# Kernel tuning notes

Measured on AMD Instinct MI355X. Metric: run time of the kernel, lower is better.

Reference implementation:

```python
import jax, jax.numpy as jnp
import numpy as np

HID = 64
HEADS = 4
HEAD_DIM = HID // HEADS
N_MOL, N_PROT = 2048, 4096
E_MOL, E_PROT = 32768, 131072
B = 32


def _lin(key, din, dout):
    kw, kb = jax.random.split(key)
    s = 1.0 / np.sqrt(din)
    W = jax.random.uniform(kw, (din, dout), jnp.float32, -s, s)
    b = jax.random.uniform(kb, (dout,), jnp.float32, -s, s)
    return W, b


def setup_inputs() -> dict:
    key = jax.random.key(0)
    ks = jax.random.split(key, 32)
    inp = {}
    inp['mol_x'] = jax.random.normal(ks[0], (N_MOL, 11), jnp.float32)
    inp['prot_x'] = jax.random.normal(ks[1], (N_PROT, 15), jnp.float32)
    inp['mol_eattr'] = jax.random.normal(ks[2], (E_MOL, 10), jnp.float32)
    inp['prot_eattr'] = jax.random.normal(ks[3], (E_PROT, 10), jnp.float32)
    inp['mol_edge_index'] = jax.random.randint(ks[4], (2, E_MOL), 0, N_MOL, jnp.int32)
    inp['prot_edge_index'] = jax.random.randint(ks[5], (2, E_PROT), 0, N_PROT, jnp.int32)
    inp['mol_batch'] = jnp.sort(jax.random.randint(ks[6], (N_MOL,), 0, B, jnp.int32))
    inp['prot_batch'] = jnp.sort(jax.random.randint(ks[7], (N_PROT,), 0, B, jnp.int32))
    inp['node_lin_mol_W'], inp['node_lin_mol_b'] = _lin(ks[8], 11, HID)
    inp['node_lin_prot_W'], inp['node_lin_prot_b'] = _lin(ks[9], 15, HID)
    inp['edge_lin_mol_W'], inp['edge_lin_mol_b'] = _lin(ks[10], 10, HID)
    inp['edge_lin_prot_W'], inp['edge_lin_prot_b'] = _lin(ks[11], 10, HID)
    for pref, base in (('mol_conv', 12), ('prot_conv', 15)):
        W1s, b1s, W2s, b2s = [], [], [], []
        for l in range(3):
            k1, k2 = jax.random.split(ks[base + l])
            W1, b1 = _lin(k1, HID, HID)
            W2, b2 = _lin(k2, HID, HID)
            W1s.append(W1); b1s.append(b1); W2s.append(W2); b2s.append(b2)
        inp[pref + '_W1'] = jnp.stack(W1s); inp[pref + '_b1'] = jnp.stack(b1s)
        inp[pref + '_W2'] = jnp.stack(W2s); inp[pref + '_b2'] = jnp.stack(b2s)
    for pref, base in (('attn_mp', 18), ('attn_pm', 21)):
        Ws, bs = [], []
        for i in range(3):  # Q, K, V
            W, b = _lin(ks[base + i], HID, HID)
            Ws.append(W); bs.append(b)
        inp[pref + '_W'] = jnp.stack(Ws); inp[pref + '_b'] = jnp.stack(bs)
    inp['fc1_W'], inp['fc1_b'] = _lin(ks[24], 2 * HID, HID)
    inp['fc2_W'], inp['fc2_b'] = _lin(ks[25], HID, 1)
    return inp


def _gine_layer(x, src, dst, eattr, W1, b1, W2, b2):
    # message: ReLU(x_j + e_ji); GINEConv sum aggregation; eps = 0
    msg = jax.nn.relu(x[src] + eattr)                       # [E, H]
    agg = jax.ops.segment_sum(msg, dst, num_segments=x.shape[0])
    h = x + agg
    h = jax.nn.relu(h @ W1 + b1) @ W2 + b2                  # inner MLP
    return jax.nn.relu(h)                                   # post-conv ReLU


def _cross_attn(qn, kn, W, b):
    Nq, Nk = qn.shape[0], kn.shape[0]
    Q = (qn @ W[0] + b[0]).reshape(Nq, HEADS, HEAD_DIM)
    K = (kn @ W[1] + b[1]).reshape(Nk, HEADS, HEAD_DIM)
    V = (kn @ W[2] + b[2]).reshape(Nk, HEADS, HEAD_DIM)
    scores = jnp.einsum('qhd,khd->hqk', Q, K) / np.sqrt(HEAD_DIM)
    w = jax.nn.softmax(scores, axis=-1)
    out = jnp.einsum('hqk,khd->qhd', w, V)
    return out.reshape(Nq, HID)


def _pool(H, batch):
    s = jax.ops.segment_sum(H, batch, num_segments=B)
    c = jax.ops.segment_sum(jnp.ones((H.shape[0],), H.dtype), batch, num_segments=B)
    return s / jnp.maximum(c, 1.0)[:, None]


def _forward(mol_x, prot_x, mol_eattr, prot_eattr,
             node_lin_mol_W, node_lin_mol_b, node_lin_prot_W, node_lin_prot_b,
             edge_lin_mol_W, edge_lin_mol_b, edge_lin_prot_W, edge_lin_prot_b,
             mol_conv_W1, mol_conv_b1, mol_conv_W2, mol_conv_b2,
             prot_conv_W1, prot_conv_b1, prot_conv_W2, prot_conv_b2,
             attn_mp_W, attn_mp_b, attn_pm_W, attn_pm_b,
             fc1_W, fc1_b, fc2_W, fc2_b,
             mol_edge_index, prot_edge_index, mol_batch, prot_batch):
    xm = mol_x @ node_lin_mol_W + node_lin_mol_b
    xp = prot_x @ node_lin_prot_W + node_lin_prot_b
    em = mol_eattr @ edge_lin_mol_W + edge_lin_mol_b
    ep = prot_eattr @ edge_lin_prot_W + edge_lin_prot_b
    ms, md = mol_edge_index[0], mol_edge_index[1]
    ps, pd = prot_edge_index[0], prot_edge_index[1]
    for l in range(3):
        xm = _gine_layer(xm, ms, md, em, mol_conv_W1[l], mol_conv_b1[l], mol_conv_W2[l], mol_conv_b2[l])
    for l in range(3):
        xp = _gine_layer(xp, ps, pd, ep, prot_conv_W1[l], prot_conv_b1[l], prot_conv_W2[l], prot_conv_b2[l])
    H_mol = xm + _cross_attn(xm, xp, attn_mp_W, attn_mp_b)
    H_prot = xp + _cross_attn(xp, xm, attn_pm_W, attn_pm_b)
    z = jnp.concatenate([_pool(H_mol, mol_batch), _pool(H_prot, prot_batch)], axis=1)
    h = jax.nn.relu(z @ fc1_W + fc1_b)
    return jax.nn.sigmoid(h @ fc2_W + fc2_b).squeeze(-1)


def reference(mol_x, prot_x, mol_eattr, prot_eattr,
              node_lin_mol_W, node_lin_mol_b, node_lin_prot_W, node_lin_prot_b,
              edge_lin_mol_W, edge_lin_mol_b, edge_lin_prot_W, edge_lin_prot_b,
              mol_conv_W1, mol_conv_b1, mol_conv_W2, mol_conv_b2,
              prot_conv_W1, prot_conv_b1, prot_conv_W2, prot_conv_b2,
              attn_mp_W, attn_mp_b, attn_pm_W, attn_pm_b,
              fc1_W, fc1_b, fc2_W, fc2_b,
              mol_edge_index, prot_edge_index, mol_batch, prot_batch):
    return _forward(mol_x, prot_x, mol_eattr, prot_eattr,
                    node_lin_mol_W, node_lin_mol_b, node_lin_prot_W, node_lin_prot_b,
                    edge_lin_mol_W, edge_lin_mol_b, edge_lin_prot_W, edge_lin_prot_b,
                    mol_conv_W1, mol_conv_b1, mol_conv_W2, mol_conv_b2,
                    prot_conv_W1, prot_conv_b1, prot_conv_W2, prot_conv_b2,
                    attn_mp_W, attn_mp_b, attn_pm_W, attn_pm_b,
                    fc1_W, fc1_b, fc2_W, fc2_b,
                    mol_edge_index, prot_edge_index, mol_batch, prot_batch)
```

## Files before the change

### kernel.cpp

```cpp
#include <hip/hip_runtime.h>
#include <math.h>

#define HID 64
#define HEADS 4
#define HDIM 16
#define N_MOL 2048
#define N_PROT 4096
#define E_MOL 32768
#define E_PROT 131072
#define BATCH 32
#define N_TOT (N_MOL + N_PROT)
#define E_TOT (E_MOL + E_PROT)
#define CAP 128

#define TQA 16
#define TKA 32
#define KSTA 68
#define CH_MOL 4
#define CH_PROT 2
#define KCHUNK 1024
#define NGRP_MOL (N_MOL / TQA)

#define DOT4(a, b) ((a).x*(b).x + (a).y*(b).y + (a).z*(b).z + (a).w*(b).w)
#define EXP2(x) __builtin_amdgcn_exp2f(x)

__global__ void k_nlb(const float* __restrict__ mol_x, const float* __restrict__ prot_x,
                      const float* __restrict__ Wm, const float* __restrict__ bm,
                      const float* __restrict__ Wp, const float* __restrict__ bp,
                      const int* __restrict__ mol_ei, const int* __restrict__ prot_ei,
                      float* __restrict__ xm, float* __restrict__ xp,
                      int* __restrict__ cursor, int* __restrict__ eidx) {
    if (blockIdx.x < N_TOT / 4) {
        int w = threadIdx.x >> 6, t = threadIdx.x & 63;
        int n = blockIdx.x * 4 + w;
        if (n < N_MOL) {
            const float* xr = mol_x + n * 11;
            float acc = bm[t];
#pragma unroll
            for (int i = 0; i < 11; ++i) acc += xr[i] * Wm[i * HID + t];
            xm[n * HID + t] = acc;
        } else {
            int p = n - N_MOL;
            const float* xr = prot_x + p * 15;
            float acc = bp[t];
#pragma unroll
            for (int i = 0; i < 15; ++i) acc += xr[i] * Wp[i * HID + t];
            xp[p * HID + t] = acc;
        }
    } else {
        int e = (blockIdx.x - N_TOT / 4) * 256 + threadIdx.x;
        int node, loc;
        if (e < E_MOL) { node = mol_ei[E_MOL + e]; loc = e; }
        else { int el = e - E_MOL; node = N_MOL + prot_ei[E_PROT + el]; loc = el; }
        int pos = atomicAdd(&cursor[node], 1);
        eidx[(size_t)node * CAP + pos] = loc;
    }
}

__global__ void k_gine(const float* __restrict__ xin_m, const float* __restrict__ xin_p,
                       float* __restrict__ xout_m, float* __restrict__ xout_p,
                       const float* __restrict__ mol_ea, const float* __restrict__ prot_ea,
                       const int* __restrict__ mol_ei, const int* __restrict__ prot_ei,
                       const float* __restrict__ Wem, const float* __restrict__ bem,
                       const float* __restrict__ Wep, const float* __restrict__ bep,
                       const float* __restrict__ W1m, const float* __restrict__ b1m,
                       const float* __restrict__ W2m, const float* __restrict__ b2m,
                       const float* __restrict__ W1p, const float* __restrict__ b1p,
                       const float* __restrict__ W2p, const float* __restrict__ b2p,
                       const int* __restrict__ cnt, const int* __restrict__ eidx,
                       int doProj,
                       const float* __restrict__ mpW, const float* __restrict__ mpb,
                       const float* __restrict__ pmW, const float* __restrict__ pmb,
                       float* __restrict__ Qm, float* __restrict__ Kp, float* __restrict__ Vp,
                       float* __restrict__ Qp, float* __restrict__ Km, float* __restrict__ Vm) {
    __shared__ float h0[8][HID];
    __shared__ float h1[8][HID];
    int w = threadIdx.x >> 6, t = threadIdx.x & 63;
    int nb0 = blockIdx.x * 8 + w * 2;
    bool isMol = nb0 < N_MOL;
    const float* x  = isMol ? xin_m : xin_p;
    float* xo       = isMol ? xout_m : xout_p;
    const float* We = isMol ? Wem : Wep;
    float bt        = isMol ? bem[t] : bep[t];
    const float* ea_base = isMol ? mol_ea : prot_ea;
    const int* srcarr    = isMol ? mol_ei : prot_ei;
    int nbias = isMol ? 0 : N_MOL;
    float wcol[10];
#pragma unroll
    for (int i = 0; i < 10; ++i) wcol[i] = We[i * HID + t];

#pragma unroll
    for (int u = 0; u < 2; ++u) {
        int nb = nb0 + u;
        int deg = cnt[nb];
        const int* lst = eidx + (size_t)nb * CAP;
        float agg = 0.f;
        int j = 0;
        for (; j + 1 < deg; j += 2) {
            int e0 = lst[j], e1 = lst[j + 1];
            int s0 = srcarr[e0], s1 = srcarr[e1];
            const float2* p0 = (const float2*)(ea_base + (size_t)e0 * 10);
            const float2* p1 = (const float2*)(ea_base + (size_t)e1 * 10);
            float2 a0 = p0[0], a1 = p0[1], a2 = p0[2], a3 = p0[3], a4 = p0[4];
            float2 c0 = p1[0], c1 = p1[1], c2 = p1[2], c3 = p1[3], c4 = p1[4];
            float xs0 = x[s0 * HID + t];
            float xs1 = x[s1 * HID + t];
            float m0 = bt, m1 = bt;
            m0 = fmaf(a0.x, wcol[0], m0); m0 = fmaf(a0.y, wcol[1], m0);
            m0 = fmaf(a1.x, wcol[2], m0); m0 = fmaf(a1.y, wcol[3], m0);
            m0 = fmaf(a2.x, wcol[4], m0); m0 = fmaf(a2.y, wcol[5], m0);
            m0 = fmaf(a3.x, wcol[6], m0); m0 = fmaf(a3.y, wcol[7], m0);
            m0 = fmaf(a4.x, wcol[8], m0); m0 = fmaf(a4.y, wcol[9], m0);
            m1 = fmaf(c0.x, wcol[0], m1); m1 = fmaf(c0.y, wcol[1], m1);
            m1 = fmaf(c1.x, wcol[2], m1); m1 = fmaf(c1.y, wcol[3], m1);
            m1 = fmaf(c2.x, wcol[4], m1); m1 = fmaf(c2.y, wcol[5], m1);
            m1 = fmaf(c3.x, wcol[6], m1); m1 = fmaf(c3.y, wcol[7], m1);
            m1 = fmaf(c4.x, wcol[8], m1); m1 = fmaf(c4.y, wcol[9], m1);
            agg += fmaxf(m0 + xs0, 0.f) + fmaxf(m1 + xs1, 0.f);
        }
        if (j < deg) {
            int e0 = lst[j];
            int s0 = srcarr[e0];
            const float2* p0 = (const float2*)(ea_base + (size_t)e0 * 10);
            float2 a0 = p0[0], a1 = p0[1], a2 = p0[2], a3 = p0[3], a4 = p0[4];
            float xs0 = x[s0 * HID + t];
            float m0 = bt;
            m0 = fmaf(a0.x, wcol[0], m0); m0 = fmaf(a0.y, wcol[1], m0);
            m0 = fmaf(a1.x, wcol[2], m0); m0 = fmaf(a1.y, wcol[3], m0);
            m0 = fmaf(a2.x, wcol[4], m0); m0 = fmaf(a2.y, wcol[5], m0);
            m0 = fmaf(a3.x, wcol[6], m0); m0 = fmaf(a3.y, wcol[7], m0);
            m0 = fmaf(a4.x, wcol[8], m0); m0 = fmaf(a4.y, wcol[9], m0);
            agg += fmaxf(m0 + xs0, 0.f);
        }
        h0[w * 2 + u][t] = x[(nb0 - nbias + u) * HID + t] + agg;
    }

    const float* W1 = isMol ? W1m : W1p;
    const float* W2 = isMol ? W2m : W2p;
    float b1v = isMol ? b1m[t] : b1p[t];
    float b2v = isMol ? b2m[t] : b2p[t];
    float acc0 = b1v, acc1 = b1v;
    const float4* hA = (const float4*)h0[w * 2];
    const float4* hB = (const float4*)h0[w * 2 + 1];
#pragma unroll
    for (int k = 0; k < 16; ++k) {
        float4 a = hA[k], b = hB[k];
        float w0 = W1[(4 * k + 0) * HID + t], w1 = W1[(4 * k + 1) * HID + t];
        float w2 = W1[(4 * k + 2) * HID + t], w3 = W1[(4 * k + 3) * HID + t];
        acc0 = fmaf(a.x, w0, acc0); acc1 = fmaf(b.x, w0, acc1);
        acc0 = fmaf(a.y, w1, acc0); acc1 = fmaf(b.y, w1, acc1);
        acc0 = fmaf(a.z, w2, acc0); acc1 = fmaf(b.z, w2, acc1);
        acc0 = fmaf(a.w, w3, acc0); acc1 = fmaf(b.w, w3, acc1);
    }
    h1[w * 2][t] = fmaxf(acc0, 0.f);
    h1[w * 2 + 1][t] = fmaxf(acc1, 0.f);
    float d0 = b2v, d1 = b2v;
    const float4* gA = (const float4*)h1[w * 2];
    const float4* gB = (const float4*)h1[w * 2 + 1];
#pragma unroll
    for (int k = 0; k < 16; ++k) {
        float4 a = gA[k], b = gB[k];
        float w0 = W2[(4 * k + 0) * HID + t], w1 = W2[(4 * k + 1) * HID + t];
        float w2 = W2[(4 * k + 2) * HID + t], w3 = W2[(4 * k + 3) * HID + t];
        d0 = fmaf(a.x, w0, d0); d1 = fmaf(b.x, w0, d1);
        d0 = fmaf(a.y, w1, d0); d1 = fmaf(b.y, w1, d1);
        d0 = fmaf(a.z, w2, d0); d1 = fmaf(b.z, w2, d1);
        d0 = fmaf(a.w, w3, d0); d1 = fmaf(b.w, w3, d1);
    }
    int n0 = nb0 - nbias;
    float xv0 = fmaxf(d0, 0.f), xv1 = fmaxf(d1, 0.f);
    xo[n0 * HID + t] = xv0;
    xo[(n0 + 1) * HID + t] = xv1;

    if (doProj) {
        h0[w * 2][t] = xv0;
        h0[w * 2 + 1][t] = xv1;
        const float *WQ, *bQ, *WK, *bK, *WV, *bV;
        float *dQ, *dK, *dV;
        if (isMol) { WQ = mpW;        bQ = mpb;       WK = pmW + 4096; bK = pmb + 64;
                     WV = pmW + 8192; bV = pmb + 128; dQ = Qm; dK = Km; dV = Vm; }
        else       { WQ = pmW;        bQ = pmb;       WK = mpW + 4096; bK = mpb + 64;
                     WV = mpW + 8192; bV = mpb + 128; dQ = Qp; dK = Kp; dV = Vp; }
        float aQ0 = bQ[t], aQ1 = aQ0;
        float aK0 = bK[t], aK1 = aK0;
        float aV0 = bV[t], aV1 = aV0;
        const float4* rA = (const float4*)h0[w * 2];
        const float4* rB = (const float4*)h0[w * 2 + 1];
#pragma unroll
        for (int k = 0; k < 16; ++k) {
            float4 a = rA[k], b = rB[k];
#pragma unroll
            for (int j = 0; j < 4; ++j) {
                float av = (j == 0) ? a.x : (j == 1) ? a.y : (j == 2) ? a.z : a.w;
                float bv = (j == 0) ? b.x : (j == 1) ? b.y : (j == 2) ? b.z : b.w;
                float wq = WQ[(4 * k + j) * HID + t];
                float wk = WK[(4 * k + j) * HID + t];
                float wv = WV[(4 * k + j) * HID + t];
                aQ0 = fmaf(av, wq, aQ0); aQ1 = fmaf(bv, wq, aQ1);
                aK0 = fmaf(av, wk, aK0); aK1 = fmaf(bv, wk, aK1);
                aV0 = fmaf(av, wv, aV0); aV1 = fmaf(bv, wv, aV1);
            }
        }
        dQ[n0 * HID + t] = aQ0; dQ[(n0 + 1) * HID + t] = aQ1;
        dK[n0 * HID + t] = aK0; dK[(n0 + 1) * HID + t] = aK1;
        dV[n0 * HID + t] = aV0; dV[(n0 + 1) * HID + t] = aV1;
    }
}

__device__ inline void upd4(float4& A, const float4 v0, const float4 v1,
                            float p0, float p1, float al) {
    A.x = fmaf(p1, v1.x, fmaf(p0, v0.x, A.x * al));
    A.y = fmaf(p1, v1.y, fmaf(p0, v0.y, A.y * al));
    A.z = fmaf(p1, v1.z, fmaf(p0, v0.z, A.z * al));
    A.w = fmaf(p1, v1.w, fmaf(p0, v0.w, A.w * al));
}
__device__ inline void merge4(float4& A, const float4 B, float c1, float c2) {
    A.x = A.x * c1 + B.x * c2;
    A.y = A.y * c1 + B.y * c2;
    A.z = A.z * c1 + B.z * c2;
    A.w = A.w * c1 + B.w * c2;
}
__device__ inline float4 shfl4(const float4 a, int off) {
    float4 r;
    r.x = __shfl_xor(a.x, off, 64); r.y = __shfl_xor(a.y, off, 64);
    r.z = __shfl_xor(a.z, off, 64); r.w = __shfl_xor(a.w, off, 64);
    return r;
}

__global__ __launch_bounds__(256) void k_attn(
    const float* __restrict__ Qm, const float* __restrict__ Kp, const float* __restrict__ Vp,
    const float* __restrict__ Qp, const float* __restrict__ Km, const float* __restrict__ Vm,
    float* __restrict__ part_m, float* __restrict__ part_p) {
    __shared__ float Kl[2][TKA * KSTA];
    __shared__ float Vl[2][TKA * KSTA];

    int t = threadIdx.x;
    const float *Q, *K, *V;
    float* part;
    int q0, chunk, CH;
    {
        int b = blockIdx.x;
        const int MOLB = NGRP_MOL * CH_MOL;
        if (b < MOLB) {
            chunk = b & 3; q0 = (b >> 2) * TQA; CH = CH_MOL;
            Q = Qm; K = Kp; V = Vp; part = part_m;
        } else {
            b -= MOLB;
            chunk = b & 1; q0 = (b >> 1) * TQA; CH = CH_PROT;
            Q = Qp; K = Km; V = Vm; part = part_p;
        }
    }
    int kbeg = chunk * KCHUNK;

    int sub = t & 15, h = (t >> 4) & 3, qg = t >> 6;
    int r0 = t >> 4;
    int c0 = (t & 15) << 2;

    const float sc = 0.25f * 1.44269504088896f;
    float4 q4[4][4];
#pragma unroll
    for (int qq = 0; qq < 4; ++qq) {
        const float4* Qr = (const float4*)(Q + (q0 + qg * 4 + qq) * HID + h * HDIM);
#pragma unroll
        for (int j = 0; j < 4; ++j) {
            float4 v = Qr[j];
            v.x *= sc; v.y *= sc; v.z *= sc; v.w *= sc;
            q4[qq][j] = v;
        }
    }

    float mreg[4], lreg[4];
    float4 A[4][4];
#pragma unroll
    for (int qq = 0; qq < 4; ++qq) {
        mreg[qq] = -INFINITY; lreg[qq] = 0.f;
#pragma unroll
        for (int j = 0; j < 4; ++j) A[qq][j] = (float4){0.f, 0.f, 0.f, 0.f};
    }

    {
        const float4* Kg = (const float4*)(K + kbeg * HID);
        const float4* Vg = (const float4*)(V + kbeg * HID);
        float4 ka = Kg[t], kb = Kg[t + 256];
        float4 va = Vg[t], vb = Vg[t + 256];
        *(float4*)&Kl[0][r0 * KSTA + c0] = ka;
        *(float4*)&Kl[0][(r0 + 16) * KSTA + c0] = kb;
        *(float4*)&Vl[0][r0 * KSTA + c0] = va;
        *(float4*)&Vl[0][(r0 + 16) * KSTA + c0] = vb;
    }
    __syncthreads();

    const int NT = KCHUNK / TKA;
    for (int tile = 0; tile < NT; ++tile) {
        int cur = tile & 1;
        float4 ka, kb, va, vb;
        bool more = (tile + 1) < NT;
        if (more) {
            const float4* Kg = (const float4*)(K + (kbeg + (tile + 1) * TKA) * HID);
            const float4* Vg = (const float4*)(V + (kbeg + (tile + 1) * TKA) * HID);
            ka = Kg[t]; kb = Kg[t + 256];
            va = Vg[t]; vb = Vg[t + 256];
        }

        const float4* Kr0 = (const float4*)&Kl[cur][sub * KSTA + h * HDIM];
        const float4* Kr1 = (const float4*)&Kl[cur][(sub + 16) * KSTA + h * HDIM];
        float4 x0 = Kr0[0], x1 = Kr0[1], x2 = Kr0[2], x3 = Kr0[3];
        float4 y0 = Kr1[0], y1 = Kr1[1], y2 = Kr1[2], y3 = Kr1[3];

        float s0[4], s1[4];
#pragma unroll
        for (int qq = 0; qq < 4; ++qq) {
            s0[qq] = DOT4(x0, q4[qq][0]) + DOT4(x1, q4[qq][1]) + DOT4(x2, q4[qq][2]) + DOT4(x3, q4[qq][3]);
            s1[qq] = DOT4(y0, q4[qq][0]) + DOT4(y1, q4[qq][1]) + DOT4(y2, q4[qq][2]) + DOT4(y3, q4[qq][3]);
        }

        const float4* Vr0 = (const float4*)&Vl[cur][sub * KSTA + h * HDIM];
        const float4* Vr1 = (const float4*)&Vl[cur][(sub + 16) * KSTA + h * HDIM];
        float4 v00 = Vr0[0], v01 = Vr0[1], v02 = Vr0[2], v03 = Vr0[3];
        float4 v10 = Vr1[0], v11 = Vr1[1], v12 = Vr1[2], v13 = Vr1[3];

#pragma unroll
        for (int qq = 0; qq < 4; ++qq) {
            float mn = fmaxf(mreg[qq], fmaxf(s0[qq], s1[qq]));
            float al = EXP2(mreg[qq] - mn);
            float p0 = EXP2(s0[qq] - mn);
            float p1 = EXP2(s1[qq] - mn);
            lreg[qq] = lreg[qq] * al + p0 + p1;
            upd4(A[qq][0], v00, v10, p0, p1, al);
            upd4(A[qq][1], v01, v11, p0, p1, al);
            upd4(A[qq][2], v02, v12, p0, p1, al);
            upd4(A[qq][3], v03, v13, p0, p1, al);
            mreg[qq] = mn;
        }

        if (more) {
            int nxt = cur ^ 1;
            *(float4*)&Kl[nxt][r0 * KSTA + c0] = ka;
            *(float4*)&Kl[nxt][(r0 + 16) * KSTA + c0] = kb;
            *(float4*)&Vl[nxt][r0 * KSTA + c0] = va;
            *(float4*)&Vl[nxt][(r0 + 16) * KSTA + c0] = vb;
        }
        __syncthreads();
    }

#pragma unroll
    for (int off = 1; off < 16; off <<= 1) {
#pragma unroll
        for (int qq = 0; qq < 4; ++qq) {
            float m2 = __shfl_xor(mreg[qq], off, 64);
            float l2 = __shfl_xor(lreg[qq], off, 64);
            float4 B0 = shfl4(A[qq][0], off), B1 = shfl4(A[qq][1], off);
            float4 B2 = shfl4(A[qq][2], off), B3 = shfl4(A[qq][3], off);
            float mn = fmaxf(mreg[qq], m2);
            float c1 = EXP2(mreg[qq] - mn), c2 = EXP2(m2 - mn);
            lreg[qq] = lreg[qq] * c1 + l2 * c2;
            merge4(A[qq][0], B0, c1, c2); merge4(A[qq][1], B1, c1, c2);
            merge4(A[qq][2], B2, c1, c2); merge4(A[qq][3], B3, c1, c2);
            mreg[qq] = mn;
        }
    }

    if (sub == 0) {
#pragma unroll
        for (int qq = 0; qq < 4; ++qq) {
            int qi = q0 + qg * 4 + qq;
            float* pp = part + (size_t)((qi * HEADS + h) * CH + chunk) * 20;
            pp[0] = mreg[qq]; pp[1] = lreg[qq];
            *(float4*)&pp[4] = A[qq][0]; *(float4*)&pp[8] = A[qq][1];
            *(float4*)&pp[12] = A[qq][2]; *(float4*)&pp[16] = A[qq][3];
        }
    }
}

__global__ void k_pool(const float* __restrict__ part_m, const float* __restrict__ part_p,
                       const float* __restrict__ xm, const float* __restrict__ xp,
                       const int* __restrict__ mb, const int* __restrict__ pb,
                       float* __restrict__ pool, float* __restrict__ cnt) {
    __shared__ float sm[64][65];
    int b = blockIdx.x >> 3, sl = blockIdx.x & 7;
    int t = threadIdx.x;
    int h = t & 3, s = t >> 2;
    int ms, me, ps, pe;
    {
        int lo = 0, hi = N_MOL;
        while (lo < hi) { int mid = (lo + hi) >> 1; if (mb[mid] < b) lo = mid + 1; else hi = mid; }
        ms = lo; lo = ms; hi = N_MOL;
        while (lo < hi) { int mid = (lo + hi) >> 1; if (mb[mid] < b + 1) lo = mid + 1; else hi = mid; }
        me = lo;
        lo = 0; hi = N_PROT;
        while (lo < hi) { int mid = (lo + hi) >> 1; if (pb[mid] < b) lo = mid + 1; else hi = mid; }
        ps = lo; lo = ps; hi = N_PROT;
        while (lo < hi) { int mid = (lo + hi) >> 1; if (pb[mid] < b + 1) lo = mid + 1; else hi = mid; }
        pe = lo;
    }
    if (sl == 0 && t == 0) { cnt[b * 2] = (float)(me - ms); cnt[b * 2 + 1] = (float)(pe - ps); }

    {
        float acc[16];
#pragma unroll
        for (int d = 0; d < 16; ++d) acc[d] = 0.f;
        for (int q = ms + sl + 8 * s; q < me; q += 8 * 64) {
            const float* p0 = part_m + (size_t)(q * HEADS + h) * CH_MOL * 20;
            float mmax = -INFINITY;
#pragma unroll
            for (int c = 0; c < CH_MOL; ++c) mmax = fmaxf(mmax, p0[c * 20]);
            float lsum = 0.f, wgt[CH_MOL];
#pragma unroll
            for (int c = 0; c < CH_MOL; ++c) {
                wgt[c] = EXP2(p0[c * 20] - mmax);
                lsum += p0[c * 20 + 1] * wgt[c];
            }
            float inv = 1.f / lsum;
            const float* Xr = xm + q * HID + h * HDIM;
#pragma unroll
            for (int d = 0; d < 16; ++d) {
                float o = Xr[d];
#pragma unroll
                for (int c = 0; c < CH_MOL; ++c)
                    o = fmaf(p0[c * 20 + 4 + d], wgt[c] * inv, o);
                acc[d] += o;
            }
        }
#pragma unroll
        for (int d = 0; d < 16; ++d) sm[s][h * 16 + d] = acc[d];
    }
    __syncthreads();
    if (t < 64) {
        float sum = 0.f;
        for (int ss = 0; ss < 64; ++ss) sum += sm[ss][t];
        unsafeAtomicAdd(&pool[b * 128 + t], sum);
    }
    __syncthreads();

    {
        float acc[16];
#pragma unroll
        for (int d = 0; d < 16; ++d) acc[d] = 0.f;
        for (int q = ps + sl + 8 * s; q < pe; q += 8 * 64) {
            const float* p0 = part_p + (size_t)(q * HEADS + h) * CH_PROT * 20;
            float m0 = p0[0], m1 = p0[20];
            float mmax = fmaxf(m0, m1);
            float w0 = EXP2(m0 - mmax), w1 = EXP2(m1 - mmax);
            float inv = 1.f / (p0[1] * w0 + p0[21] * w1);
            w0 *= inv; w1 *= inv;
            const float* Xr = xp + q * HID + h * HDIM;
#pragma unroll
            for (int d = 0; d < 16; ++d)
                acc[d] += Xr[d] + p0[4 + d] * w0 + p0[24 + d] * w1;
        }
#pragma unroll
        for (int d = 0; d < 16; ++d) sm[s][h * 16 + d] = acc[d];
    }
    __syncthreads();
    if (t < 64) {
        float sum = 0.f;
        for (int ss = 0; ss < 64; ++ss) sum += sm[ss][t];
        unsafeAtomicAdd(&pool[b * 128 + 64 + t], sum);
    }
}

__global__ void k_head(const float* __restrict__ pool, const float* __restrict__ cnt,
                       const float* __restrict__ fc1W, const float* __restrict__ fc1b,
                       const float* __restrict__ fc2W, const float* __restrict__ fc2b,
                       float* __restrict__ out) {
    __shared__ float z[128];
    int b = blockIdx.x, t = threadIdx.x;
    float cm = fmaxf(cnt[b * 2 + 0], 1.f), cp = fmaxf(cnt[b * 2 + 1], 1.f);
    z[t] = pool[b * 128 + t] / cm;
    z[64 + t] = pool[b * 128 + 64 + t] / cp;
    __syncthreads();
    float acc = fc1b[t];
    const float4* zv = (const float4*)z;
#pragma unroll
    for (int k = 0; k < 32; ++k) {
        float4 hv = zv[k];
        acc = fmaf(hv.x, fc1W[(4 * k + 0) * 64 + t], acc);
        acc = fmaf(hv.y, fc1W[(4 * k + 1) * 64 + t], acc);
        acc = fmaf(hv.z, fc1W[(4 * k + 2) * 64 + t], acc);
        acc = fmaf(hv.w, fc1W[(4 * k + 3) * 64 + t], acc);
    }
    float hv = fmaxf(acc, 0.f);
    float prod = hv * fc2W[t];
#pragma unroll
    for (int off = 32; off > 0; off >>= 1) prod += __shfl_xor(prod, off, 64);
    if (t == 0) out[b] = 1.f / (1.f + __expf(-(prod + fc2b[0])));
}

extern "C" void kernel_launch(void* const* d_in, const int* in_sizes, int n_in,
                              void* d_out, int out_size, void* d_ws, size_t ws_size,
                              hipStream_t stream) {
    const float* mol_x   = (const float*)d_in[0];
    const float* prot_x  = (const float*)d_in[1];
    const float* mol_ea  = (const float*)d_in[2];
    const float* prot_ea = (const float*)d_in[3];
    const int*   mol_ei  = (const int*)d_in[4];
    const int*   prot_ei = (const int*)d_in[5];
    const int*   mol_b   = (const int*)d_in[6];
    const int*   prot_b  = (const int*)d_in[7];
    const float* nlmW = (const float*)d_in[8];
    const float* nlmb = (const float*)d_in[9];
    const float* nlpW = (const float*)d_in[10];
    const float* nlpb = (const float*)d_in[11];
    const float* elmW = (const float*)d_in[12];
    const float* elmb = (const float*)d_in[13];
    const float* elpW = (const float*)d_in[14];
    const float* elpb = (const float*)d_in[15];
    const float* mcW1 = (const float*)d_in[16];
    const float* mcb1 = (const float*)d_in[17];
    const float* mcW2 = (const float*)d_in[18];
    const float* mcb2 = (const float*)d_in[19];
    const float* pcW1 = (const float*)d_in[20];
    const float* pcb1 = (const float*)d_in[21];
    const float* pcW2 = (const float*)d_in[22];
    const float* pcb2 = (const float*)d_in[23];
    const float* mpW  = (const float*)d_in[24];
    const float* mpb  = (const float*)d_in[25];
    const float* pmW  = (const float*)d_in[26];
    const float* pmb  = (const float*)d_in[27];
    const float* fc1W = (const float*)d_in[28];
    const float* fc1b = (const float*)d_in[29];
    const float* fc2W = (const float*)d_in[30];
    const float* fc2b = (const float*)d_in[31];

    float* ws    = (float*)d_ws;
    float* xa_m  = ws;
    float* xa_p  = xa_m + 131072;
    float* xb_m  = xa_p + 262144;
    float* xb_p  = xb_m + 131072;
    float* Qm    = xb_p + 262144;
    float* Kp    = Qm + 131072;
    float* Vp    = Kp + 262144;
    float* Qp    = Vp + 262144;
    float* Km    = Qp + 262144;
    float* Vm    = Km + 131072;
    float* partm = Vm + 131072;
    float* partp = partm + 655360;
    int* cursor  = (int*)(partp + 655360);
    float* pool  = (float*)(cursor + N_TOT);
    float* cnt   = pool + 4096;
    int* eidx    = (int*)partm;

    hipMemsetAsync(cursor, 0, (size_t)(N_TOT + 4096 + 64) * 4, stream);

    k_nlb<<<N_TOT / 4 + E_TOT / 256, 256, 0, stream>>>(
        mol_x, prot_x, nlmW, nlmb, nlpW, nlpb, mol_ei, prot_ei, xa_m, xa_p, cursor, eidx);

    k_gine<<<N_TOT / 8, 256, 0, stream>>>(xa_m, xa_p, xb_m, xb_p, mol_ea, prot_ea, mol_ei, prot_ei,
        elmW, elmb, elpW, elpb,
        mcW1, mcb1, mcW2, mcb2, pcW1, pcb1, pcW2, pcb2, cursor, eidx,
        0, mpW, mpb, pmW, pmb, Qm, Kp, Vp, Qp, Km, Vm);
    k_gine<<<N_TOT / 8, 256, 0, stream>>>(xb_m, xb_p, xa_m, xa_p, mol_ea, prot_ea, mol_ei, prot_ei,
        elmW, elmb, elpW, elpb,
        mcW1 + 4096, mcb1 + 64, mcW2 + 4096, mcb2 + 64,
        pcW1 + 4096, pcb1 + 64, pcW2 + 4096, pcb2 + 64, cursor, eidx,
        0, mpW, mpb, pmW, pmb, Qm, Kp, Vp, Qp, Km, Vm);
    k_gine<<<N_TOT / 8, 256, 0, stream>>>(xa_m, xa_p, xb_m, xb_p, mol_ea, prot_ea, mol_ei, prot_ei,
        elmW, elmb, elpW, elpb,
        mcW1 + 8192, mcb1 + 128, mcW2 + 8192, mcb2 + 128,
        pcW1 + 8192, pcb1 + 128, pcW2 + 8192, pcb2 + 128, cursor, eidx,
        1, mpW, mpb, pmW, pmb, Qm, Kp, Vp, Qp, Km, Vm);

    k_attn<<<NGRP_MOL * CH_MOL + (N_PROT / TQA) * CH_PROT, 256, 0, stream>>>(
        Qm, Kp, Vp, Qp, Km, Vm, partm, partp);

    k_pool<<<BATCH * 8, 256, 0, stream>>>(partm, partp, xb_m, xb_p, mol_b, prot_b, pool, cnt);
    k_head<<<BATCH, 64, 0, stream>>>(pool, cnt, fc1W, fc1b, fc2W, fc2b, (float*)d_out);
}
```

Before: 371.4 us.

## Replace CSR-style gather aggregation with edge-parallel atomic scatter kernels

Drops the per-destination edge bucket build, which used atomic cursors and capacity-bounded lists. Each GINE layer is split into an edge-parallel message kernel that scatters with float atomics into an aggregation buffer, plus a node kernel that reads and zeroes that buffer before its MLP. This removes the serial per-node loop over neighbour lists and the bucketing pass. In exchange it adds heavy atomic traffic per layer, two more kernel launches, and an order-dependent float summation.

```diff
diff --git a/kernel.cpp b/kernel.cpp
--- a/kernel.cpp
+++ b/kernel.cpp
@@ -11,7 +11,6 @@
 #define BATCH 32
 #define N_TOT (N_MOL + N_PROT)
 #define E_TOT (E_MOL + E_PROT)
-#define CAP 128
 
 #define TQA 16
 #define TKA 32
@@ -21,53 +20,86 @@
 #define KCHUNK 1024
 #define NGRP_MOL (N_MOL / TQA)
 
+#define EPW 4
+
 #define DOT4(a, b) ((a).x*(b).x + (a).y*(b).y + (a).z*(b).z + (a).w*(b).w)
 #define EXP2(x) __builtin_amdgcn_exp2f(x)
 
-__global__ void k_nlb(const float* __restrict__ mol_x, const float* __restrict__ prot_x,
-                      const float* __restrict__ Wm, const float* __restrict__ bm,
-                      const float* __restrict__ Wp, const float* __restrict__ bp,
-                      const int* __restrict__ mol_ei, const int* __restrict__ prot_ei,
-                      float* __restrict__ xm, float* __restrict__ xp,
-                      int* __restrict__ cursor, int* __restrict__ eidx) {
-    if (blockIdx.x < N_TOT / 4) {
-        int w = threadIdx.x >> 6, t = threadIdx.x & 63;
-        int n = blockIdx.x * 4 + w;
-        if (n < N_MOL) {
-            const float* xr = mol_x + n * 11;
-            float acc = bm[t];
-#pragma unroll
-            for (int i = 0; i < 11; ++i) acc += xr[i] * Wm[i * HID + t];
-            xm[n * HID + t] = acc;
-        } else {
-            int p = n - N_MOL;
-            const float* xr = prot_x + p * 15;
-            float acc = bp[t];
-#pragma unroll
-            for (int i = 0; i < 15; ++i) acc += xr[i] * Wp[i * HID + t];
-            xp[p * HID + t] = acc;
-        }
+__global__ void k_nl(const float* __restrict__ mol_x, const float* __restrict__ prot_x,
+                     const float* __restrict__ Wm, const float* __restrict__ bm,
+                     const float* __restrict__ Wp, const float* __restrict__ bp,
+                     float* __restrict__ xm, float* __restrict__ xp) {
+    int w = threadIdx.x >> 6, t = threadIdx.x & 63;
+    int n = blockIdx.x * 4 + w;
+    if (n < N_MOL) {
+        const float* xr = mol_x + n * 11;
+        float acc = bm[t];
+#pragma unroll
+        for (int i = 0; i < 11; ++i) acc += xr[i] * Wm[i * HID + t];
+        xm[n * HID + t] = acc;
     } else {
-        int e = (blockIdx.x - N_TOT / 4) * 256 + threadIdx.x;
-        int node, loc;
-        if (e < E_MOL) { node = mol_ei[E_MOL + e]; loc = e; }
-        else { int el = e - E_MOL; node = N_MOL + prot_ei[E_PROT + el]; loc = el; }
-        int pos = atomicAdd(&cursor[node], 1);
-        eidx[(size_t)node * CAP + pos] = loc;
-    }
-}
-
-__global__ void k_gine(const float* __restrict__ xin_m, const float* __restrict__ xin_p,
+        int p = n - N_MOL;
+        const float* xr = prot_x + p * 15;
+        float acc = bp[t];
+#pragma unroll
+        for (int i = 0; i < 15; ++i) acc += xr[i] * Wp[i * HID + t];
+        xp[p * HID + t] = acc;
+    }
+}
+
+__global__ __launch_bounds__(256) void k_msg(
+    const float* __restrict__ xm, const float* __restrict__ xp,
+    const float* __restrict__ mol_ea, const float* __restrict__ prot_ea,
+    const int* __restrict__ mol_ei, const int* __restrict__ prot_ei,
+    const float* __restrict__ Wem, const float* __restrict__ bem,
+    const float* __restrict__ Wep, const float* __restrict__ bep,
+    float* __restrict__ agg_m, float* __restrict__ agg_p) {
+    int t = threadIdx.x & 63, w = threadIdx.x >> 6;
+    int eb = blockIdx.x * (4 * EPW) + w * EPW;
+    const float* x; const float* ea; const int* ei;
+    const float* We; const float* be; float* agg; int E;
+    if (eb < E_MOL) {
+        x = xm; ea = mol_ea; ei = mol_ei; We = Wem; be = bem; agg = agg_m; E = E_MOL;
+    } else {
+        eb -= E_MOL;
+        x = xp; ea = prot_ea; ei = prot_ei; We = Wep; be = bep; agg = agg_p; E = E_PROT;
+    }
+    float bt = be[t];
+    float wcol[10];
+#pragma unroll
+    for (int i = 0; i < 10; ++i) wcol[i] = We[i * HID + t];
+
+    int s[EPW], d[EPW];
+    float2 a[EPW][5];
+#pragma unroll
+    for (int i = 0; i < EPW; ++i) {
+        int e = eb + i;
+        s[i] = ei[e];
+        d[i] = ei[E + e];
+        const float2* p = (const float2*)(ea + (size_t)e * 10);
+#pragma unroll
+        for (int j = 0; j < 5; ++j) a[i][j] = p[j];
+    }
+#pragma unroll
+    for (int i = 0; i < EPW; ++i) {
+        float m = bt;
+#pragma unroll
+        for (int j = 0; j < 5; ++j) {
+            m = fmaf(a[i][j].x, wcol[2 * j], m);
+            m = fmaf(a[i][j].y, wcol[2 * j + 1], m);
+        }
+        float msg = fmaxf(m + x[(size_t)s[i] * HID + t], 0.f);
+        unsafeAtomicAdd(&agg[(size_t)d[i] * HID + t], msg);
+    }
+}
+
+__global__ void k_node(const float* __restrict__ xin_m, const float* __restrict__ xin_p,
                        float* __restrict__ xout_m, float* __restrict__ xout_p,
-                       const float* __restrict__ mol_ea, const float* __restrict__ prot_ea,
-                       const int* __restrict__ mol_ei, const int* __restrict__ prot_ei,
-                       const float* __restrict__ Wem, const float* __restrict__ bem,
-                       const float* __restrict__ Wep, const float* __restrict__ bep,
+                       float* __restrict__ agg_m, float* __restrict__ agg_p,
                        const float* __restrict__ W1m, const float* __restrict__ b1m,
                        const float* __restrict__ W2m, const float* __restrict__ b2m,
                        const float* __restrict__ W1p, const float* __restrict__ b1p,
                        const float* __restrict__ W2p, const float* __restrict__ b2p,
-                       const int* __restrict__ cnt, const int* __restrict__ eidx,
                        int doProj,
                        const float* __restrict__ mpW, const float* __restrict__ mpb,
                        const float* __restrict__ pmW, const float* __restrict__ pmb,
@@ -80,59 +112,15 @@
     bool isMol = nb0 < N_MOL;
     const float* x  = isMol ? xin_m : xin_p;
     float* xo       = isMol ? xout_m : xout_p;
-    const float* We = isMol ? Wem : Wep;
-    float bt        = isMol ? bem[t] : bep[t];
-    const float* ea_base = isMol ? mol_ea : prot_ea;
-    const int* srcarr    = isMol ? mol_ei : prot_ei;
+    float* agg      = isMol ? agg_m : agg_p;
     int nbias = isMol ? 0 : N_MOL;
-    float wcol[10];
-#pragma unroll
-    for (int i = 0; i < 10; ++i) wcol[i] = We[i * HID + t];
+    int n0 = nb0 - nbias;
 
 #pragma unroll
     for (int u = 0; u < 2; ++u) {
-        int nb = nb0 + u;
-        int deg = cnt[nb];
-        const int* lst = eidx + (size_t)nb * CAP;
-        float agg = 0.f;
-        int j = 0;
-        for (; j + 1 < deg; j += 2) {
-            int e0 = lst[j], e1 = lst[j + 1];
-            int s0 = srcarr[e0], s1 = srcarr[e1];
-            const float2* p0 = (const float2*)(ea_base + (size_t)e0 * 10);
-            const float2* p1 = (const float2*)(ea_base + (size_t)e1 * 10);
-            float2 a0 = p0[0], a1 = p0[1], a2 = p0[2], a3 = p0[3], a4 = p0[4];
-            float2 c0 = p1[0], c1 = p1[1], c2 = p1[2], c3 = p1[3], c4 = p1[4];
-            float xs0 = x[s0 * HID + t];
-            float xs1 = x[s1 * HID + t];
-            float m0 = bt, m1 = bt;
-            m0 = fmaf(a0.x, wcol[0], m0); m0 = fmaf(a0.y, wcol[1], m0);
-            m0 = fmaf(a1.x, wcol[2], m0); m0 = fmaf(a1.y, wcol[3], m0);
-            m0 = fmaf(a2.x, wcol[4], m0); m0 = fmaf(a2.y, wcol[5], m0);
-            m0 = fmaf(a3.x, wcol[6], m0); m0 = fmaf(a3.y, wcol[7], m0);
-            m0 = fmaf(a4.x, wcol[8], m0); m0 = fmaf(a4.y, wcol[9], m0);
-            m1 = fmaf(c0.x, wcol[0], m1); m1 = fmaf(c0.y, wcol[1], m1);
-            m1 = fmaf(c1.x, wcol[2], m1); m1 = fmaf(c1.y, wcol[3], m1);
-            m1 = fmaf(c2.x, wcol[4], m1); m1 = fmaf(c2.y, wcol[5], m1);
-            m1 = fmaf(c3.x, wcol[6], m1); m1 = fmaf(c3.y, wcol[7], m1);
-            m1 = fmaf(c4.x, wcol[8], m1); m1 = fmaf(c4.y, wcol[9], m1);
-            agg += fmaxf(m0 + xs0, 0.f) + fmaxf(m1 + xs1, 0.f);
-        }
-        if (j < deg) {
-            int e0 = lst[j];
-            int s0 = srcarr[e0];
-            const float2* p0 = (const float2*)(ea_base + (size_t)e0 * 10);
-            float2 a0 = p0[0], a1 = p0[1], a2 = p0[2], a3 = p0[3], a4 = p0[4];
-            float xs0 = x[s0 * HID + t];
-            float m0 = bt;
-            m0 = fmaf(a0.x, wcol[0], m0); m0 = fmaf(a0.y, wcol[1], m0);
-            m0 = fmaf(a1.x, wcol[2], m0); m0 = fmaf(a1.y, wcol[3], m0);
-            m0 = fmaf(a2.x, wcol[4], m0); m0 = fmaf(a2.y, wcol[5], m0);
-            m0 = fmaf(a3.x, wcol[6], m0); m0 = fmaf(a3.y, wcol[7], m0);
-            m0 = fmaf(a4.x, wcol[8], m0); m0 = fmaf(a4.y, wcol[9], m0);
-            agg += fmaxf(m0 + xs0, 0.f);
-        }
-        h0[w * 2 + u][t] = x[(nb0 - nbias + u) * HID + t] + agg;
+        size_t idx = (size_t)(n0 + u) * HID + t;
+        h0[w * 2 + u][t] = x[idx] + agg[idx];
+        agg[idx] = 0.f;
     }
 
     const float* W1 = isMol ? W1m : W1p;
@@ -167,7 +155,6 @@
         d0 = fmaf(a.z, w2, d0); d1 = fmaf(b.z, w2, d1);
         d0 = fmaf(a.w, w3, d0); d1 = fmaf(b.w, w3, d1);
     }
-    int n0 = nb0 - nbias;
     float xv0 = fmaxf(d0, 0.f), xv1 = fmaxf(d1, 0.f);
     xo[n0 * HID + t] = xv0;
     xo[(n0 + 1) * HID + t] = xv1;
@@ -535,29 +522,32 @@
     float* Vm    = Km + 131072;
     float* partm = Vm + 131072;
     float* partp = partm + 655360;
-    int* cursor  = (int*)(partp + 655360);
-    float* pool  = (float*)(cursor + N_TOT);
+    float* pool  = partp + 655360;
     float* cnt   = pool + 4096;
-    int* eidx    = (int*)partm;
-
-    hipMemsetAsync(cursor, 0, (size_t)(N_TOT + 4096 + 64) * 4, stream);
-
-    k_nlb<<<N_TOT / 4 + E_TOT / 256, 256, 0, stream>>>(
-        mol_x, prot_x, nlmW, nlmb, nlpW, nlpb, mol_ei, prot_ei, xa_m, xa_p, cursor, eidx);
-
-    k_gine<<<N_TOT / 8, 256, 0, stream>>>(xa_m, xa_p, xb_m, xb_p, mol_ea, prot_ea, mol_ei, prot_ei,
-        elmW, elmb, elpW, elpb,
-        mcW1, mcb1, mcW2, mcb2, pcW1, pcb1, pcW2, pcb2, cursor, eidx,
+    float* agg_m = partm;
+    float* agg_p = partm + 131072;
+
+    hipMemsetAsync(pool, 0, (size_t)(4096 + 64) * 4, stream);
+    hipMemsetAsync(agg_m, 0, (size_t)(131072 + 262144) * 4, stream);
+
+    k_nl<<<N_TOT / 4, 256, 0, stream>>>(mol_x, prot_x, nlmW, nlmb, nlpW, nlpb, xa_m, xa_p);
+
+    k_msg<<<E_TOT / (4 * EPW), 256, 0, stream>>>(xa_m, xa_p, mol_ea, prot_ea, mol_ei, prot_ei,
+        elmW, elmb, elpW, elpb, agg_m, agg_p);
+    k_node<<<N_TOT / 8, 256, 0, stream>>>(xa_m, xa_p, xb_m, xb_p, agg_m, agg_p,
+        mcW1, mcb1, mcW2, mcb2, pcW1, pcb1, pcW2, pcb2,
         0, mpW, mpb, pmW, pmb, Qm, Kp, Vp, Qp, Km, Vm);
-    k_gine<<<N_TOT / 8, 256, 0, stream>>>(xb_m, xb_p, xa_m, xa_p, mol_ea, prot_ea, mol_ei, prot_ei,
-        elmW, elmb, elpW, elpb,
+    k_msg<<<E_TOT / (4 * EPW), 256, 0, stream>>>(xb_m, xb_p, mol_ea, prot_ea, mol_ei, prot_ei,
+        elmW, elmb, elpW, elpb, agg_m, agg_p);
+    k_node<<<N_TOT / 8, 256, 0, stream>>>(xb_m, xb_p, xa_m, xa_p, agg_m, agg_p,
         mcW1 + 4096, mcb1 + 64, mcW2 + 4096, mcb2 + 64,
-        pcW1 + 4096, pcb1 + 64, pcW2 + 4096, pcb2 + 64, cursor, eidx,
+        pcW1 + 4096, pcb1 + 64, pcW2 + 4096, pcb2 + 64,
         0, mpW, mpb, pmW, pmb, Qm, Kp, Vp, Qp, Km, Vm);
-    k_gine<<<N_TOT / 8, 256, 0, stream>>>(xa_m, xa_p, xb_m, xb_p, mol_ea, prot_ea, mol_ei, prot_ei,
-        elmW, elmb, elpW, elpb,
+    k_msg<<<E_TOT / (4 * EPW), 256, 0, stream>>>(xa_m, xa_p, mol_ea, prot_ea, mol_ei, prot_ei,
+        elmW, elmb, elpW, elpb, agg_m, agg_p);
+    k_node<<<N_TOT / 8, 256, 0, stream>>>(xa_m, xa_p, xb_m, xb_p, agg_m, agg_p,
         mcW1 + 8192, mcb1 + 128, mcW2 + 8192, mcb2 + 128,
-        pcW1 + 8192, pcb1 + 128, pcW2 + 8192, pcb2 + 128, cursor, eidx,
+        pcW1 + 8192, pcb1 + 128, pcW2 + 8192, pcb2 + 128,
         1, mpW, mpb, pmW, pmb, Qm, Kp, Vp, Qp, Km, Vm);
 
     k_attn<<<NGRP_MOL * CH_MOL + (N_PROT / TQA) * CH_PROT, 256, 0, stream>>>(
```

New measurement: 371.8 us. About the same (+0.1%).
